# Kernel tuning notes

Measured on AMD Instinct MI355X. Metric: run time of the kernel, lower is better.

## Reference

```python
import jax, jax.numpy as jnp
import numpy as np

EPS = 1e-12
HEADS = 16
DIM_KEYS = 16
DIM_VALUES = 64


def l2norm(t):
    # matches F.normalize(t, p=2, dim=-1) with eps=1e-12
    n = jnp.linalg.norm(t, axis=-1, keepdims=True)
    return t / jnp.maximum(n, EPS)


def tanh_norm(t):
    n = jnp.linalg.norm(t, axis=-1, keepdims=True)
    return jnp.tanh(n) * (t / jnp.maximum(n, EPS))


def split_heads(x, h):
    # [b, n, h*d] -> [b, h, n, d]
    b, n, hd = x.shape
    return x.reshape(b, n, h, hd // h).transpose(0, 2, 1, 3)


def setup_inputs() -> dict:
    key = jax.random.key(0)
    k1, k2, k3, k4 = jax.random.split(key, 4)
    b, n, dim = 4, 2048, 1024
    dim_inner = (DIM_KEYS + DIM_VALUES) * HEADS  # 1280
    tokens = jax.random.normal(k1, (b, n, dim), dtype=jnp.float32)
    Wqg = jax.random.normal(k2, (dim, dim_inner), dtype=jnp.float32) * (dim ** -0.5)
    Wkv = jax.random.normal(k3, (dim, dim_inner), dtype=jnp.float32) * (dim ** -0.5)
    Wout = jax.random.normal(k4, (DIM_VALUES * HEADS, dim), dtype=jnp.float32) * ((DIM_VALUES * HEADS) ** -0.5)
    return {"tokens": tokens, "Wqg": Wqg, "Wkv": Wkv, "Wout": Wout}


def reference(tokens, Wqg, Wkv, Wout):
    # self-attention variant: context = tokens, mask = None
    qg = split_heads(tokens @ Wqg, HEADS)   # [b, h, n, dk+dv]
    kv = split_heads(tokens @ Wkv, HEADS)
    queries, gates = qg[..., :DIM_KEYS], qg[..., DIM_KEYS:]
    keys, values = kv[..., :DIM_KEYS], kv[..., DIM_KEYS:]
    queries, keys, values = l2norm(queries), l2norm(keys), l2norm(values)
    sim = jnp.einsum('bhid,bhjd->bhij', queries, keys)
    attn = jnp.square(jax.nn.relu(sim))
    aggr = jnp.einsum('bhij,bhjd->bhid', attn, values)
    out = tanh_norm(aggr) * jnp.tanh(jax.nn.silu(gates))
    b, h, n, d = out.shape
    out = out.transpose(0, 2, 1, 3).reshape(b, n, h * d)  # merge heads
    return out @ Wout
```

## Files before the change

### kernel.cpp

```cpp
#include <hip/hip_runtime.h>
#include <cstdint>
#include <cstddef>

typedef __attribute__((ext_vector_type(8))) short short8;
typedef __attribute__((ext_vector_type(8))) unsigned short ushort8;
typedef __attribute__((ext_vector_type(4))) float f32x4;
typedef __attribute__((ext_vector_type(8))) _Float16 half8;
typedef __attribute__((ext_vector_type(4))) _Float16 half4;
typedef __attribute__((ext_vector_type(2))) __fp16 fp16x2;

#define DEV static __device__ __forceinline__

DEV unsigned short f2bf(float x) {
  union { float f; unsigned u; } v; v.f = x;
  unsigned r = v.u + 0x7fffu + ((v.u >> 16) & 1u);
  return (unsigned short)(r >> 16);
}
DEV unsigned pack2bf(float lo, float hi) {
  union { float f; unsigned u; } a, b; a.f = lo; b.f = hi;
  return __builtin_amdgcn_perm(b.u + 0x8000u, a.u + 0x8000u, 0x07060302u);
}
DEV f32x4 mfma16(short8 a, short8 b, f32x4 c) {
  return __builtin_amdgcn_mfma_f32_16x16x32_bf16(a, b, c, 0, 0, 0);
}
DEV f32x4 mfma16h(half8 a, half8 b, f32x4 c) {
  return __builtin_amdgcn_mfma_f32_16x16x32_f16(a, b, c, 0, 0, 0);
}
DEV f32x4 mfma16k(half4 a, half4 b, f32x4 c) {
  return __builtin_amdgcn_mfma_f32_16x16x16f16(a, b, c, 0, 0, 0);
}

typedef __attribute__((address_space(1))) unsigned int g_u32;
typedef __attribute__((address_space(3))) unsigned int l_u32;
DEV void glds16(const unsigned short* g, unsigned short* l) {
  __builtin_amdgcn_global_load_lds((g_u32*)g, (l_u32*)l, 16, 0, 0);
}

constexpr int Bc = 4, Nc = 2048, Dc = 1024, Hc = 16, DKc = 16, DVc = 64, DIc = 1280;
constexpr int Mc = Bc * Nc;

__global__ __launch_bounds__(256) void prep_kernel(const float* __restrict__ X,
                                                   unsigned short* __restrict__ Xb,
                                                   const float* __restrict__ Wqg,
                                                   unsigned short* __restrict__ WqgT,
                                                   const float* __restrict__ Wkv,
                                                   unsigned short* __restrict__ WkvT,
                                                   const float* __restrict__ Wout,
                                                   unsigned short* __restrict__ WoutT) {
  __shared__ unsigned short tsh[64][72];
  int bid = blockIdx.x, tid = threadIdx.x;
  if (bid < 4096) {
    int i = bid * 256 + tid;
    const float4* p = (const float4*)(X + (size_t)i * 8);
    float4 a = p[0], b = p[1];
    ushort8 o;
    o[0] = f2bf(a.x); o[1] = f2bf(a.y); o[2] = f2bf(a.z); o[3] = f2bf(a.w);
    o[4] = f2bf(b.x); o[5] = f2bf(b.y); o[6] = f2bf(b.z); o[7] = f2bf(b.w);
    *(ushort8*)(Xb + (size_t)i * 8) = o;
    return;
  }
  const float* W; unsigned short* WT; int K, N, tb;
  if (bid < 4416)      { W = Wqg;  WT = WqgT;  K = Dc; N = DIc; tb = bid - 4096; }
  else if (bid < 4736) { W = Wkv;  WT = WkvT;  K = Dc; N = DIc; tb = bid - 4416; }
  else                 { W = Wout; WT = WoutT; K = Dc; N = Dc;  tb = bid - 4736; }
  int k0 = (tb & 15) * 64, n0 = (tb >> 4) * 64;
#pragma unroll
  for (int it = 0; it < 16; ++it) {
    int f = it * 256 + tid;
    int r = f >> 6, c = f & 63;
    tsh[c][r] = f2bf(W[(size_t)(k0 + r) * N + n0 + c]);
  }
  __syncthreads();
#pragma unroll
  for (int it = 0; it < 16; ++it) {
    int f = it * 256 + tid;
    int r = f >> 6, c = f & 63;
    WT[(size_t)(n0 + r) * K + k0 + c] = tsh[r][c];
  }
}

__global__ __launch_bounds__(256) void gemm_proj(const unsigned short* __restrict__ A,
                                                 const unsigned short* __restrict__ BT,
                                                 unsigned short* __restrict__ QG,
                                                 unsigned short* __restrict__ KV,
                                                 int Kq) {
  __shared__ unsigned short As[128 * 64];
  __shared__ unsigned short Bs[128 * 64];
  int L = blockIdx.x;
  int xcd = L & 7, idx = L >> 3;
  int brow = xcd * 8 + (idx & 7);
  int bcol = idx >> 3;
  int row0 = brow * 128, col0 = bcol * 128;
  int tid = threadIdx.x, lane = tid & 63, wave = tid >> 6;
  int wm = wave >> 1, wn = wave & 1;
  int ql = lane >> 4, l16 = lane & 15;
  int r8 = lane >> 3, cbl = (lane & 7) ^ r8;

  unsigned short* dst = (col0 >= DIc) ? KV : QG;
  int c0l = (col0 >= DIc) ? col0 - DIc : col0;

  const unsigned short* gA = A + (size_t)(row0 + wave * 32 + r8) * Kq + cbl * 8;
  const unsigned short* gB = BT + (size_t)(col0 + wave * 32 + r8) * Kq + cbl * 8;

  f32x4 acc[4][4];
#pragma unroll
  for (int i = 0; i < 4; i++)
#pragma unroll
    for (int j = 0; j < 4; j++) acc[i][j] = (f32x4){0.f, 0.f, 0.f, 0.f};

  for (int k0 = 0; k0 < Kq; k0 += 64) {
    __syncthreads();
#pragma unroll
    for (int i = 0; i < 4; ++i) {
      glds16(gA + (size_t)(i * 8) * Kq + k0, &As[(wave * 32 + i * 8) * 64]);
      glds16(gB + (size_t)(i * 8) * Kq + k0, &Bs[(wave * 32 + i * 8) * 64]);
    }
    __syncthreads();
#pragma unroll
    for (int kk = 0; kk < 64; kk += 32) {
      short8 af[4], bfr[4];
#pragma unroll
      for (int t = 0; t < 4; t++) {
        int row = wm * 64 + t * 16 + l16;
        int cb = (kk >> 3) + ql;
        af[t] = *(const short8*)&As[row * 64 + ((cb ^ (row & 7)) << 3)];
      }
#pragma unroll
      for (int t = 0; t < 4; t++) {
        int row = wn * 64 + t * 16 + l16;
        int cb = (kk >> 3) + ql;
        bfr[t] = *(const short8*)&Bs[row * 64 + ((cb ^ (row & 7)) << 3)];
      }
#pragma unroll
      for (int i = 0; i < 4; i++)
#pragma unroll
        for (int j = 0; j < 4; j++) acc[i][j] = mfma16(af[i], bfr[j], acc[i][j]);
    }
  }
#pragma unroll
  for (int i = 0; i < 4; i++)
#pragma unroll
    for (int j = 0; j < 4; j++)
#pragma unroll
      for (int r = 0; r < 4; r++) {
        int rr = row0 + wm * 64 + i * 16 + ql * 4 + r;
        int cc = c0l + wn * 64 + j * 16 + l16;
        union { _Float16 h; unsigned short us; } cv;
        cv.h = (_Float16)acc[i][j][r];
        dst[(size_t)rr * DIc + cc] = cv.us;
      }
}

__global__ __launch_bounds__(256) void gemm_glds(const unsigned short* __restrict__ A,
                                                 const unsigned short* __restrict__ BT,
                                                 float* __restrict__ Cout,
                                                 int Mq, int Nq, int Kq) {
  __shared__ unsigned short As[128 * 64];
  __shared__ unsigned short Bs[128 * 64];
  int L = blockIdx.x;
  int xcd = L & 7, idx = L >> 3;
  int brow = xcd * 8 + (idx & 7);
  int bcol = idx >> 3;
  int row0 = brow * 128, col0 = bcol * 128;
  int tid = threadIdx.x, lane = tid & 63, wave = tid >> 6;
  int wm = wave >> 1, wn = wave & 1;
  int ql = lane >> 4, l16 = lane & 15;
  int r8 = lane >> 3, cbl = (lane & 7) ^ r8;

  const unsigned short* gA = A + (size_t)(row0 + wave * 32 + r8) * Kq + cbl * 8;
  const unsigned short* gB = BT + (size_t)(col0 + wave * 32 + r8) * Kq + cbl * 8;

  f32x4 acc[4][4];
#pragma unroll
  for (int i = 0; i < 4; i++)
#pragma unroll
    for (int j = 0; j < 4; j++) acc[i][j] = (f32x4){0.f, 0.f, 0.f, 0.f};

  for (int k0 = 0; k0 < Kq; k0 += 64) {
    __syncthreads();
#pragma unroll
    for (int i = 0; i < 4; ++i) {
      glds16(gA + (size_t)(i * 8) * Kq + k0, &As[(wave * 32 + i * 8) * 64]);
      glds16(gB + (size_t)(i * 8) * Kq + k0, &Bs[(wave * 32 + i * 8) * 64]);
    }
    __syncthreads();
#pragma unroll
    for (int kk = 0; kk < 64; kk += 32) {
      short8 af[4], bfr[4];
#pragma unroll
      for (int t = 0; t < 4; t++) {
        int row = wm * 64 + t * 16 + l16;
        int cb = (kk >> 3) + ql;
        af[t] = *(const short8*)&As[row * 64 + ((cb ^ (row & 7)) << 3)];
      }
#pragma unroll
      for (int t = 0; t < 4; t++) {
        int row = wn * 64 + t * 16 + l16;
        int cb = (kk >> 3) + ql;
        bfr[t] = *(const short8*)&Bs[row * 64 + ((cb ^ (row & 7)) << 3)];
      }
#pragma unroll
      for (int i = 0; i < 4; i++)
#pragma unroll
        for (int j = 0; j < 4; j++) acc[i][j] = mfma16(af[i], bfr[j], acc[i][j]);
    }
  }
#pragma unroll
  for (int i = 0; i < 4; i++)
#pragma unroll
    for (int j = 0; j < 4; j++)
#pragma unroll
      for (int r = 0; r < 4; r++) {
        int rr = row0 + wm * 64 + i * 16 + ql * 4 + r;
        int cc = col0 + wn * 64 + j * 16 + l16;
        Cout[(size_t)rr * Nq + cc] = acc[i][j][r];
      }
}

__global__ __launch_bounds__(256) void norm_kernel(const unsigned short* __restrict__ QG,
                                                   const unsigned short* __restrict__ KV,
                                                   unsigned short* __restrict__ Qn,
                                                   unsigned short* __restrict__ Kn,
                                                   unsigned short* __restrict__ Vtg)
{
  int g = blockIdx.x * 256 + threadIdx.x;
  int n = g & (Nc - 1), bh = g >> 11;
  int h = bh & 15, b = bh >> 4;
  size_t src = ((size_t)(b * Nc + n)) * DIc + h * 80;

  {
    half8 u0 = *(const half8*)&QG[src];
    half8 u1 = *(const half8*)&QG[src + 8];
    float q[16], ss = 0.f;
#pragma unroll
    for (int i = 0; i < 8; i++) { q[i] = (float)u0[i]; q[8 + i] = (float)u1[i]; }
#pragma unroll
    for (int i = 0; i < 16; i++) ss += q[i] * q[i];
    float sc = 1.f / fmaxf(sqrtf(ss), 1e-12f);
    half8 o0, o1;
#pragma unroll
    for (int i = 0; i < 8; i++) { o0[i] = (_Float16)(q[i] * sc); o1[i] = (_Float16)(q[8 + i] * sc); }
    size_t dst = ((size_t)bh * Nc + n) * 16;
    *(half8*)&Qn[dst] = o0;
    *(half8*)&Qn[dst + 8] = o1;
  }
  {
    half8 u0 = *(const half8*)&KV[src];
    half8 u1 = *(const half8*)&KV[src + 8];
    float q[16], ss = 0.f;
#pragma unroll
    for (int i = 0; i < 8; i++) { q[i] = (float)u0[i]; q[8 + i] = (float)u1[i]; }
#pragma unroll
    for (int i = 0; i < 16; i++) ss += q[i] * q[i];
    float sc = 1.f / fmaxf(sqrtf(ss), 1e-12f);
    half8 o0, o1;
#pragma unroll
    for (int i = 0; i < 8; i++) { o0[i] = (_Float16)(q[i] * sc); o1[i] = (_Float16)(q[8 + i] * sc); }
    size_t dst = ((size_t)bh * Nc + n) * 16;
    *(half8*)&Kn[dst] = o0;
    *(half8*)&Kn[dst + 8] = o1;
  }
  {
    half8 u[8];
#pragma unroll
    for (int i = 0; i < 8; i++) u[i] = *(const half8*)&KV[src + 16 + i * 8];
    float ss = 0.f;
#pragma unroll
    for (int i = 0; i < 8; i++)
#pragma unroll
      for (int j = 0; j < 8; j++) { float x = (float)u[i][j]; ss += x * x; }
    float sc = 1.f / fmaxf(sqrtf(ss), 1e-12f);
#pragma unroll
    for (int i = 0; i < 8; i++)
#pragma unroll
      for (int j = 0; j < 8; j++) {
        int d = i * 8 + j;
        union { _Float16 h; unsigned short us; } cv;
        cv.h = (_Float16)((float)u[i][j] * sc);
        Vtg[((size_t)bh * DVc + d) * Nc + n] = cv.us;
      }
  }
}

__global__ __launch_bounds__(256, 4) void attn_kernel(const unsigned short* __restrict__ Qn,
                                                      const unsigned short* __restrict__ Kn,
                                                      const unsigned short* __restrict__ Vtg,
                                                      const unsigned short* __restrict__ QG,
                                                      unsigned short* __restrict__ outpre) {
  __shared__ unsigned short shm[2 * 64 * 128];

  int gid = blockIdx.x;
  int xcd = gid & 7, slot = gid >> 3;
  int bh = xcd * 8 + (slot & 7);
  int q0 = (slot >> 3) * 128;
  int b = bh >> 4, h = bh & 15;
  int tid = threadIdx.x, lane = tid & 63, wave = tid >> 6;
  int ql = lane >> 4, l16 = lane & 15;
  int qw0 = q0 + wave * 32;

  half4 qf[2];
#pragma unroll
  for (int qt = 0; qt < 2; ++qt)
    qf[qt] = *(const half4*)&Qn[((size_t)bh * Nc + qw0 + qt * 16 + l16) * 16 + ql * 4];

  const unsigned short* krow = Kn + (size_t)bh * Nc * 16;
  const unsigned short* vbase = Vtg + ((size_t)bh * DVc) * Nc;

  int lq = lane >> 4, m16 = lane & 15;

  f32x4 acc[4][2];
#pragma unroll
  for (int dt = 0; dt < 4; dt++) { acc[dt][0] = (f32x4){0.f,0.f,0.f,0.f}; acc[dt][1] = (f32x4){0.f,0.f,0.f,0.f}; }

  half4 kfA[8], kfB[8];

#pragma unroll
  for (int kh = 0; kh < 8; ++kh)
    kfA[kh] = *(const half4*)&krow[(size_t)(kh * 16 + l16) * 16 + ql * 4];
#pragma unroll
  for (int i = 0; i < 4; ++i) {
    int r0 = i * 16 + wave * 4;
    int d = r0 + lq;
    glds16(vbase + (size_t)d * Nc + 0 + ((m16 ^ (d & 7)) << 3), &shm[r0 * 128]);
  }

#define TILE_BODY(KT, KFU, KFN, LN)                                                      \
  {                                                                                      \
    __syncthreads();     \
    unsigned short* vtb = &shm[((KT) & 1) * 8192];                                       \
    if (LN) {                                                                            \
      int kn0 = ((KT) + 1) * 128;                                                        \
      unsigned short* nb = &shm[(((KT) + 1) & 1) * 8192];                                \
      _Pragma("unroll") for (int i = 0; i < 4; ++i) {                                    \
        int r0 = i * 16 + wave * 4;                                                      \
        int d = r0 + lq;                                                                 \
        glds16(vbase + (size_t)d * Nc + kn0 + ((m16 ^ (d & 7)) << 3), &nb[r0 * 128]);    \
      }                                                                                  \
      _Pragma("unroll") for (int kh = 0; kh < 8; ++kh)                                   \
        KFN[kh] = *(const half4*)&krow[(size_t)(kn0 + kh * 16 + l16) * 16 + ql * 4];     \
    }                                                                                    \
    _Pragma("unroll") for (int p = 0; p < 4; ++p) {                    \
      f32x4 c0[2], c1[2];                                                                \
      _Pragma("unroll") for (int qt = 0; qt < 2; ++qt) {                                 \
        c0[qt] = mfma16k(KFU[2 * p],     qf[qt], (f32x4){0.f, 0.f, 0.f, 0.f});           \
        c1[qt] = mfma16k(KFU[2 * p + 1], qf[qt], (f32x4){0.f, 0.f, 0.f, 0.f});           \
      }                                                                                  \
      half8 pf[2];                                                                       \
      _Pragma("unroll") for (int qt = 0; qt < 2; ++qt) {                                 \
        union { half8 hh; fp16x2 p2[4]; } w;                                             \
        fp16x2 t0 = __builtin_amdgcn_cvt_pkrtz(c0[qt][0], c0[qt][1]);                    \
        fp16x2 t1 = __builtin_amdgcn_cvt_pkrtz(c0[qt][2], c0[qt][3]);                    \
        fp16x2 t2 = __builtin_amdgcn_cvt_pkrtz(c1[qt][0], c1[qt][1]);                    \
        fp16x2 t3 = __builtin_amdgcn_cvt_pkrtz(c1[qt][2], c1[qt][3]);                    \
        const fp16x2 hz = {(__fp16)0, (__fp16)0};                                        \
        t0 = __builtin_elementwise_max(t0, hz); w.p2[0] = t0 * t0;                       \
        t1 = __builtin_elementwise_max(t1, hz); w.p2[1] = t1 * t1;                       \
        t2 = __builtin_elementwise_max(t2, hz); w.p2[2] = t2 * t2;                       \
        t3 = __builtin_elementwise_max(t3, hz); w.p2[3] = t3 * t3;                       \
        pf[qt] = w.hh;                                                                   \
      }                                                                                  \
               \
      int tsw = (l16 & 7) << 1;                                                          \
      int s1 = ((p * 8 + ql) ^ tsw) << 2;                                                \
      int s2 = ((p * 8 + 4 + ql) ^ tsw) << 2;                                            \
      __builtin_amdgcn_s_setprio(1);                                                     \
      _Pragma("unroll") for (int dt = 0; dt < 4; ++dt) {                                 \
        const unsigned short* vrow = vtb + (dt * 16 + l16) * 128;                        \
        union { half8 s; uint4 u; } vf;                                                  \
        uint2 va = *(const uint2*)&vrow[s1];                                             \
        uint2 vb2 = *(const uint2*)&vrow[s2];                                            \
        vf.u.x = va.x; vf.u.y = va.y; vf.u.z = vb2.x; vf.u.w = vb2.y;                    \
        _Pragma("unroll") for (int qt = 0; qt < 2; ++qt)                                 \
          acc[dt][qt] = mfma16h(vf.s, pf[qt], acc[dt][qt]);                              \
      }                                                                                  \
      __builtin_amdgcn_s_setprio(0);                                                     \
    }                                                                                    \
  }

#pragma unroll 1
  for (int kt2 = 0; kt2 < 8; ++kt2) {
    int kte = kt2 * 2;
    TILE_BODY(kte, kfA, kfB, 1)
    TILE_BODY(kte + 1, kfB, kfA, (kt2 < 7))
  }
#undef TILE_BODY

  __syncthreads();
  unsigned short(*of)[68] = (unsigned short(*)[68])shm;

#pragma unroll
  for (int qt = 0; qt < 2; ++qt) {
    float ss = 0.f;
#pragma unroll
    for (int dt = 0; dt < 4; ++dt)
#pragma unroll
      for (int r = 0; r < 4; ++r) { float v = acc[dt][qt][r]; ss += v * v; }
    ss += __shfl_xor(ss, 16, 64);
    ss += __shfl_xor(ss, 32, 64);
    float nrm = sqrtf(ss);
    float sc = tanhf(nrm) / fmaxf(nrm, 1e-12f);
    int q = qw0 + qt * 16 + l16;
    size_t gbase = ((size_t)(b * Nc + q)) * DIc + h * 80 + DKc;
#pragma unroll
    for (int dt = 0; dt < 4; ++dt) {
      uint2 gu = *(const uint2*)&QG[gbase + dt * 16 + ql * 4];
      union { uint2 u; _Float16 h[4]; } gv; gv.u = gu;
      float o[4];
#pragma unroll
      for (int r = 0; r < 4; ++r) {
        float x = (float)gv.h[r];
        float s = x / (1.f + __expf(-x));
        float e2 = __expf(2.f * s);
        float g = 1.f - 2.f / (e2 + 1.f);
        o[r] = acc[dt][qt][r] * sc * g;
      }
      uint2 w;
      w.x = pack2bf(o[0], o[1]);
      w.y = pack2bf(o[2], o[3]);
      *(uint2*)&of[wave * 32 + qt * 16 + l16][dt * 16 + ql * 4] = w;
    }
  }
  __syncthreads();
  {
    int row = tid >> 1, cb = (tid & 1) * 32;
    size_t obase = ((size_t)(b * Nc + q0 + row)) * (Hc * DVc) + h * DVc + cb;
#pragma unroll
    for (int i = 0; i < 4; ++i)
      *(ushort8*)&outpre[obase + i * 8] = *(const ushort8*)&of[row][cb + i * 8];
  }
}

extern "C" void kernel_launch(void* const* d_in, const int* in_sizes, int n_in,
                              void* d_out, int out_size, void* d_ws, size_t ws_size,
                              hipStream_t stream) {
  const float* X = (const float*)d_in[0];
  const float* Wqg = (const float*)d_in[1];
  const float* Wkv = (const float*)d_in[2];
  const float* Wout = (const float*)d_in[3];
  float* out = (float*)d_out;
  (void)in_sizes; (void)n_in; (void)out_size; (void)ws_size;

  char* ws = (char*)d_ws;
  size_t off = 0;
  auto alloc = [&](size_t bytes) {
    void* p = ws + off;
    off += (bytes + 255) & ~(size_t)255;
    return p;
  };
  unsigned short* Xbf   = (unsigned short*)alloc((size_t)Mc * Dc * 2);
  unsigned short* WqgT  = (unsigned short*)alloc((size_t)DIc * Dc * 2);
  unsigned short* WkvT  = (unsigned short*)alloc((size_t)DIc * Dc * 2);
  unsigned short* WoutT = (unsigned short*)alloc((size_t)Dc * Dc * 2);
  unsigned short* QG    = (unsigned short*)alloc((size_t)Mc * DIc * 2);
  unsigned short* KV    = (unsigned short*)alloc((size_t)Mc * DIc * 2);
  unsigned short* Qn    = (unsigned short*)alloc((size_t)Bc * Hc * Nc * 16 * 2);
  unsigned short* Kn    = (unsigned short*)alloc((size_t)Bc * Hc * Nc * 16 * 2);
  unsigned short* Vtg   = (unsigned short*)alloc((size_t)Bc * Hc * Nc * DVc * 2);
  unsigned short* outpre = Xbf;

  prep_kernel<<<4992, 256, 0, stream>>>(X, Xbf, Wqg, WqgT, Wkv, WkvT, Wout, WoutT);
  gemm_proj<<<Mc / 128 * (2 * DIc / 128), 256, 0, stream>>>(Xbf, WqgT, QG, KV, Dc);
  norm_kernel<<<(Mc * Hc) / 256, 256, 0, stream>>>(QG, KV, Qn, Kn, Vtg);
  attn_kernel<<<1024, 256, 0, stream>>>(Qn, Kn, Vtg, QG, outpre);
  gemm_glds<<<Mc / 128 * (Dc / 128), 256, 0, stream>>>(outpre, WoutT, out, Mc, Dc, Dc);
}
```

Before: 242.0 us.

## Use 8 waves per attention block with one query tile per wave

Result: slower. 264.7 us (+9.4%).

```diff
diff --git a/kernel.cpp b/kernel.cpp
--- a/kernel.cpp
+++ b/kernel.cpp
@@ -282,7 +282,7 @@
   }
 }
 
-__global__ __launch_bounds__(256, 4) void attn_kernel(const unsigned short* __restrict__ Qn,
+__global__ __launch_bounds__(512, 8) void attn_kernel(const unsigned short* __restrict__ Qn,
                                                       const unsigned short* __restrict__ Kn,
                                                       const unsigned short* __restrict__ Vtg,
                                                       const unsigned short* __restrict__ QG,
@@ -296,136 +296,120 @@
   int b = bh >> 4, h = bh & 15;
   int tid = threadIdx.x, lane = tid & 63, wave = tid >> 6;
   int ql = lane >> 4, l16 = lane & 15;
-  int qw0 = q0 + wave * 32;
-
-  half4 qf[2];
-#pragma unroll
-  for (int qt = 0; qt < 2; ++qt)
-    qf[qt] = *(const half4*)&Qn[((size_t)bh * Nc + qw0 + qt * 16 + l16) * 16 + ql * 4];
+  int qw0 = q0 + wave * 16;
+
+  half4 qf = *(const half4*)&Qn[((size_t)bh * Nc + qw0 + l16) * 16 + ql * 4];
 
   const unsigned short* krow = Kn + (size_t)bh * Nc * 16;
   const unsigned short* vbase = Vtg + ((size_t)bh * DVc) * Nc;
 
   int lq = lane >> 4, m16 = lane & 15;
-
-  f32x4 acc[4][2];
-#pragma unroll
-  for (int dt = 0; dt < 4; dt++) { acc[dt][0] = (f32x4){0.f,0.f,0.f,0.f}; acc[dt][1] = (f32x4){0.f,0.f,0.f,0.f}; }
-
-  half4 kfA[8], kfB[8];
-
-#pragma unroll
-  for (int kh = 0; kh < 8; ++kh)
-    kfA[kh] = *(const half4*)&krow[(size_t)(kh * 16 + l16) * 16 + ql * 4];
-#pragma unroll
-  for (int i = 0; i < 4; ++i) {
-    int r0 = i * 16 + wave * 4;
+  int tsw = (l16 & 7) << 1;
+
+  f32x4 acc[4];
+#pragma unroll
+  for (int dt = 0; dt < 4; dt++) acc[dt] = (f32x4){0.f, 0.f, 0.f, 0.f};
+
+#pragma unroll
+  for (int i = 0; i < 2; ++i) {
+    int r0 = i * 32 + wave * 4;
     int d = r0 + lq;
     glds16(vbase + (size_t)d * Nc + 0 + ((m16 ^ (d & 7)) << 3), &shm[r0 * 128]);
   }
 
-#define TILE_BODY(KT, KFU, KFN, LN)                                                      \
-  {                                                                                      \
-    __syncthreads();     \
-    unsigned short* vtb = &shm[((KT) & 1) * 8192];                                       \
-    if (LN) {                                                                            \
-      int kn0 = ((KT) + 1) * 128;                                                        \
-      unsigned short* nb = &shm[(((KT) + 1) & 1) * 8192];                                \
-      _Pragma("unroll") for (int i = 0; i < 4; ++i) {                                    \
-        int r0 = i * 16 + wave * 4;                                                      \
-        int d = r0 + lq;                                                                 \
-        glds16(vbase + (size_t)d * Nc + kn0 + ((m16 ^ (d & 7)) << 3), &nb[r0 * 128]);    \
-      }                                                                                  \
-      _Pragma("unroll") for (int kh = 0; kh < 8; ++kh)                                   \
-        KFN[kh] = *(const half4*)&krow[(size_t)(kn0 + kh * 16 + l16) * 16 + ql * 4];     \
-    }                                                                                    \
-    _Pragma("unroll") for (int p = 0; p < 4; ++p) {                    \
-      f32x4 c0[2], c1[2];                                                                \
-      _Pragma("unroll") for (int qt = 0; qt < 2; ++qt) {                                 \
-        c0[qt] = mfma16k(KFU[2 * p],     qf[qt], (f32x4){0.f, 0.f, 0.f, 0.f});           \
-        c1[qt] = mfma16k(KFU[2 * p + 1], qf[qt], (f32x4){0.f, 0.f, 0.f, 0.f});           \
-      }                                                                                  \
-      half8 pf[2];                                                                       \
-      _Pragma("unroll") for (int qt = 0; qt < 2; ++qt) {                                 \
-        union { half8 hh; fp16x2 p2[4]; } w;                                             \
-        fp16x2 t0 = __builtin_amdgcn_cvt_pkrtz(c0[qt][0], c0[qt][1]);                    \
-        fp16x2 t1 = __builtin_amdgcn_cvt_pkrtz(c0[qt][2], c0[qt][3]);                    \
-        fp16x2 t2 = __builtin_amdgcn_cvt_pkrtz(c1[qt][0], c1[qt][1]);                    \
-        fp16x2 t3 = __builtin_amdgcn_cvt_pkrtz(c1[qt][2], c1[qt][3]);                    \
-        const fp16x2 hz = {(__fp16)0, (__fp16)0};                                        \
-        t0 = __builtin_elementwise_max(t0, hz); w.p2[0] = t0 * t0;                       \
-        t1 = __builtin_elementwise_max(t1, hz); w.p2[1] = t1 * t1;                       \
-        t2 = __builtin_elementwise_max(t2, hz); w.p2[2] = t2 * t2;                       \
-        t3 = __builtin_elementwise_max(t3, hz); w.p2[3] = t3 * t3;                       \
-        pf[qt] = w.hh;                                                                   \
-      }                                                                                  \
-               \
-      int tsw = (l16 & 7) << 1;                                                          \
-      int s1 = ((p * 8 + ql) ^ tsw) << 2;                                                \
-      int s2 = ((p * 8 + 4 + ql) ^ tsw) << 2;                                            \
-      __builtin_amdgcn_s_setprio(1);                                                     \
-      _Pragma("unroll") for (int dt = 0; dt < 4; ++dt) {                                 \
-        const unsigned short* vrow = vtb + (dt * 16 + l16) * 128;                        \
-        union { half8 s; uint4 u; } vf;                                                  \
-        uint2 va = *(const uint2*)&vrow[s1];                                             \
-        uint2 vb2 = *(const uint2*)&vrow[s2];                                            \
-        vf.u.x = va.x; vf.u.y = va.y; vf.u.z = vb2.x; vf.u.w = vb2.y;                    \
-        _Pragma("unroll") for (int qt = 0; qt < 2; ++qt)                                 \
-          acc[dt][qt] = mfma16h(vf.s, pf[qt], acc[dt][qt]);                              \
-      }                                                                                  \
-      __builtin_amdgcn_s_setprio(0);                                                     \
-    }                                                                                    \
-  }
-
 #pragma unroll 1
-  for (int kt2 = 0; kt2 < 8; ++kt2) {
-    int kte = kt2 * 2;
-    TILE_BODY(kte, kfA, kfB, 1)
-    TILE_BODY(kte + 1, kfB, kfA, (kt2 < 7))
-  }
-#undef TILE_BODY
+  for (int kt = 0; kt < Nc / 128; ++kt) {
+    int k0 = kt * 128;
+    unsigned short* vtb = &shm[(kt & 1) * 8192];
+    __syncthreads();
+
+    half4 kf[8];
+#pragma unroll
+    for (int kh = 0; kh < 8; ++kh)
+      kf[kh] = *(const half4*)&krow[(size_t)(k0 + kh * 16 + l16) * 16 + ql * 4];
+
+    if (kt < Nc / 128 - 1) {
+      unsigned short* nb = &shm[((kt + 1) & 1) * 8192];
+      int kn0 = k0 + 128;
+#pragma unroll
+      for (int i = 0; i < 2; ++i) {
+        int r0 = i * 32 + wave * 4;
+        int d = r0 + lq;
+        glds16(vbase + (size_t)d * Nc + kn0 + ((m16 ^ (d & 7)) << 3), &nb[r0 * 128]);
+      }
+    }
+
+    __builtin_amdgcn_s_setprio(1);
+#pragma unroll
+    for (int p = 0; p < 4; ++p) {
+      f32x4 c0 = mfma16k(kf[2 * p],     qf, (f32x4){0.f, 0.f, 0.f, 0.f});
+      f32x4 c1 = mfma16k(kf[2 * p + 1], qf, (f32x4){0.f, 0.f, 0.f, 0.f});
+      union { half8 hh; fp16x2 p2[4]; } w;
+      fp16x2 t0 = __builtin_amdgcn_cvt_pkrtz(c0[0], c0[1]);
+      fp16x2 t1 = __builtin_amdgcn_cvt_pkrtz(c0[2], c0[3]);
+      fp16x2 t2 = __builtin_amdgcn_cvt_pkrtz(c1[0], c1[1]);
+      fp16x2 t3 = __builtin_amdgcn_cvt_pkrtz(c1[2], c1[3]);
+      const fp16x2 hz = {(__fp16)0, (__fp16)0};
+      t0 = __builtin_elementwise_max(t0, hz); w.p2[0] = t0 * t0;
+      t1 = __builtin_elementwise_max(t1, hz); w.p2[1] = t1 * t1;
+      t2 = __builtin_elementwise_max(t2, hz); w.p2[2] = t2 * t2;
+      t3 = __builtin_elementwise_max(t3, hz); w.p2[3] = t3 * t3;
+      half8 pf = w.hh;
+      int s1 = ((p * 8 + ql) ^ tsw) << 2;
+      int s2 = s1 ^ 16;
+#pragma unroll
+      for (int dt = 0; dt < 4; ++dt) {
+        const unsigned short* vrow = vtb + (dt * 16 + l16) * 128;
+        union { half8 s; uint4 u; } vf;
+        uint2 va = *(const uint2*)&vrow[s1];
+        uint2 vb2 = *(const uint2*)&vrow[s2];
+        vf.u.x = va.x; vf.u.y = va.y; vf.u.z = vb2.x; vf.u.w = vb2.y;
+        acc[dt] = mfma16h(vf.s, pf, acc[dt]);
+      }
+    }
+    __builtin_amdgcn_s_setprio(0);
+  }
 
   __syncthreads();
   unsigned short(*of)[68] = (unsigned short(*)[68])shm;
 
-#pragma unroll
-  for (int qt = 0; qt < 2; ++qt) {
+  {
     float ss = 0.f;
 #pragma unroll
     for (int dt = 0; dt < 4; ++dt)
 #pragma unroll
-      for (int r = 0; r < 4; ++r) { float v = acc[dt][qt][r]; ss += v * v; }
+      for (int r = 0; r < 4; ++r) { float v = acc[dt][r]; ss += v * v; }
     ss += __shfl_xor(ss, 16, 64);
     ss += __shfl_xor(ss, 32, 64);
     float nrm = sqrtf(ss);
     float sc = tanhf(nrm) / fmaxf(nrm, 1e-12f);
-    int q = qw0 + qt * 16 + l16;
+    int q = qw0 + l16;
     size_t gbase = ((size_t)(b * Nc + q)) * DIc + h * 80 + DKc;
 #pragma unroll
     for (int dt = 0; dt < 4; ++dt) {
       uint2 gu = *(const uint2*)&QG[gbase + dt * 16 + ql * 4];
-      union { uint2 u; _Float16 h[4]; } gv; gv.u = gu;
+      union { uint2 u; _Float16 hv[4]; } gv; gv.u = gu;
       float o[4];
 #pragma unroll
       for (int r = 0; r < 4; ++r) {
-        float x = (float)gv.h[r];
+        float x = (float)gv.hv[r];
         float s = x / (1.f + __expf(-x));
         float e2 = __expf(2.f * s);
         float g = 1.f - 2.f / (e2 + 1.f);
-        o[r] = acc[dt][qt][r] * sc * g;
+        o[r] = acc[dt][r] * sc * g;
       }
       uint2 w;
       w.x = pack2bf(o[0], o[1]);
       w.y = pack2bf(o[2], o[3]);
-      *(uint2*)&of[wave * 32 + qt * 16 + l16][dt * 16 + ql * 4] = w;
+      *(uint2*)&of[wave * 16 + l16][dt * 16 + ql * 4] = w;
     }
   }
   __syncthreads();
   {
-    int row = tid >> 1, cb = (tid & 1) * 32;
+    int row = tid >> 2, cb = (tid & 3) * 16;
     size_t obase = ((size_t)(b * Nc + q0 + row)) * (Hc * DVc) + h * DVc + cb;
 #pragma unroll
-    for (int i = 0; i < 4; ++i)
+    for (int i = 0; i < 2; ++i)
       *(ushort8*)&outpre[obase + i * 8] = *(const ushort8*)&of[row][cb + i * 8];
   }
 }
@@ -461,6 +445,6 @@
   prep_kernel<<<4992, 256, 0, stream>>>(X, Xbf, Wqg, WqgT, Wkv, WkvT, Wout, WoutT);
   gemm_proj<<<Mc / 128 * (2 * DIc / 128), 256, 0, stream>>>(Xbf, WqgT, QG, KV, Dc);
   norm_kernel<<<(Mc * Hc) / 256, 256, 0, stream>>>(QG, KV, Qn, Kn, Vtg);
-  attn_kernel<<<1024, 256, 0, stream>>>(Qn, Kn, Vtg, QG, outpre);
+  attn_kernel<<<1024, 512, 0, stream>>>(Qn, Kn, Vtg, QG, outpre);
   gemm_glds<<<Mc / 128 * (Dc / 128), 256, 0, stream>>>(outpre, WoutT, out, Mc, Dc, Dc);
 }
```

## Double per-block query tile in attention to reuse K/V tiles across more queries

Applied to the files above, without the earlier changes.

Result: slower. 294.2 us (+21.6%).

```diff
diff --git a/kernel.cpp b/kernel.cpp
--- a/kernel.cpp
+++ b/kernel.cpp
@@ -282,7 +282,7 @@
   }
 }
 
-__global__ __launch_bounds__(256, 4) void attn_kernel(const unsigned short* __restrict__ Qn,
+__global__ __launch_bounds__(256, 2) void attn_kernel(const unsigned short* __restrict__ Qn,
                                                       const unsigned short* __restrict__ Kn,
                                                       const unsigned short* __restrict__ Vtg,
                                                       const unsigned short* __restrict__ QG,
@@ -292,25 +292,28 @@
   int gid = blockIdx.x;
   int xcd = gid & 7, slot = gid >> 3;
   int bh = xcd * 8 + (slot & 7);
-  int q0 = (slot >> 3) * 128;
+  int q0 = (slot >> 3) * 256;
   int b = bh >> 4, h = bh & 15;
   int tid = threadIdx.x, lane = tid & 63, wave = tid >> 6;
   int ql = lane >> 4, l16 = lane & 15;
-  int qw0 = q0 + wave * 32;
-
-  half4 qf[2];
-#pragma unroll
-  for (int qt = 0; qt < 2; ++qt)
+  int qw0 = q0 + wave * 64;
+
+  half4 qf[4];
+#pragma unroll
+  for (int qt = 0; qt < 4; ++qt)
     qf[qt] = *(const half4*)&Qn[((size_t)bh * Nc + qw0 + qt * 16 + l16) * 16 + ql * 4];
 
   const unsigned short* krow = Kn + (size_t)bh * Nc * 16;
   const unsigned short* vbase = Vtg + ((size_t)bh * DVc) * Nc;
 
   int lq = lane >> 4, m16 = lane & 15;
-
-  f32x4 acc[4][2];
-#pragma unroll
-  for (int dt = 0; dt < 4; dt++) { acc[dt][0] = (f32x4){0.f,0.f,0.f,0.f}; acc[dt][1] = (f32x4){0.f,0.f,0.f,0.f}; }
+  int tsw = (l16 & 7) << 1;
+
+  f32x4 acc[4][4];
+#pragma unroll
+  for (int dt = 0; dt < 4; dt++)
+#pragma unroll
+    for (int qt = 0; qt < 4; qt++) acc[dt][qt] = (f32x4){0.f, 0.f, 0.f, 0.f};
 
   half4 kfA[8], kfB[8];
 
@@ -339,14 +342,15 @@
       _Pragma("unroll") for (int kh = 0; kh < 8; ++kh)                                   \
         KFN[kh] = *(const half4*)&krow[(size_t)(kn0 + kh * 16 + l16) * 16 + ql * 4];     \
     }                                                                                    \
+    __builtin_amdgcn_s_setprio(1);                                                       \
     _Pragma("unroll") for (int p = 0; p < 4; ++p) {                    \
-      f32x4 c0[2], c1[2];                                                                \
-      _Pragma("unroll") for (int qt = 0; qt < 2; ++qt) {                                 \
+      f32x4 c0[4], c1[4];                                                                \
+      _Pragma("unroll") for (int qt = 0; qt < 4; ++qt) {                                 \
         c0[qt] = mfma16k(KFU[2 * p],     qf[qt], (f32x4){0.f, 0.f, 0.f, 0.f});           \
         c1[qt] = mfma16k(KFU[2 * p + 1], qf[qt], (f32x4){0.f, 0.f, 0.f, 0.f});           \
       }                                                                                  \
-      half8 pf[2];                                                                       \
-      _Pragma("unroll") for (int qt = 0; qt < 2; ++qt) {                                 \
+      half8 pf[4];                                                                       \
+      _Pragma("unroll") for (int qt = 0; qt < 4; ++qt) {                                 \
         union { half8 hh; fp16x2 p2[4]; } w;                                             \
         fp16x2 t0 = __builtin_amdgcn_cvt_pkrtz(c0[qt][0], c0[qt][1]);                    \
         fp16x2 t1 = __builtin_amdgcn_cvt_pkrtz(c0[qt][2], c0[qt][3]);                    \
@@ -359,22 +363,20 @@
         t3 = __builtin_elementwise_max(t3, hz); w.p2[3] = t3 * t3;                       \
         pf[qt] = w.hh;                                                                   \
       }                                                                                  \
-               \
-      int tsw = (l16 & 7) << 1;                                                          \
+                                      \
       int s1 = ((p * 8 + ql) ^ tsw) << 2;                                                \
-      int s2 = ((p * 8 + 4 + ql) ^ tsw) << 2;                                            \
-      __builtin_amdgcn_s_setprio(1);                                                     \
+      int s2 = s1 ^ 16;                                                                  \
       _Pragma("unroll") for (int dt = 0; dt < 4; ++dt) {                                 \
         const unsigned short* vrow = vtb + (dt * 16 + l16) * 128;                        \
         union { half8 s; uint4 u; } vf;                                                  \
         uint2 va = *(const uint2*)&vrow[s1];                                             \
         uint2 vb2 = *(const uint2*)&vrow[s2];                                            \
         vf.u.x = va.x; vf.u.y = va.y; vf.u.z = vb2.x; vf.u.w = vb2.y;                    \
-        _Pragma("unroll") for (int qt = 0; qt < 2; ++qt)                                 \
+        _Pragma("unroll") for (int qt = 0; qt < 4; ++qt)                                 \
           acc[dt][qt] = mfma16h(vf.s, pf[qt], acc[dt][qt]);                              \
       }                                                                                  \
-      __builtin_amdgcn_s_setprio(0);                                                     \
     }                                                                                    \
+    __builtin_amdgcn_s_setprio(0);                                                       \
   }
 
 #pragma unroll 1
@@ -385,48 +387,55 @@
   }
 #undef TILE_BODY
 
-  __syncthreads();
   unsigned short(*of)[68] = (unsigned short(*)[68])shm;
-
-#pragma unroll
-  for (int qt = 0; qt < 2; ++qt) {
-    float ss = 0.f;
-#pragma unroll
-    for (int dt = 0; dt < 4; ++dt)
-#pragma unroll
-      for (int r = 0; r < 4; ++r) { float v = acc[dt][qt][r]; ss += v * v; }
-    ss += __shfl_xor(ss, 16, 64);
-    ss += __shfl_xor(ss, 32, 64);
-    float nrm = sqrtf(ss);
-    float sc = tanhf(nrm) / fmaxf(nrm, 1e-12f);
-    int q = qw0 + qt * 16 + l16;
-    size_t gbase = ((size_t)(b * Nc + q)) * DIc + h * 80 + DKc;
-#pragma unroll
-    for (int dt = 0; dt < 4; ++dt) {
-      uint2 gu = *(const uint2*)&QG[gbase + dt * 16 + ql * 4];
-      union { uint2 u; _Float16 h[4]; } gv; gv.u = gu;
-      float o[4];
-#pragma unroll
-      for (int r = 0; r < 4; ++r) {
-        float x = (float)gv.h[r];
-        float s = x / (1.f + __expf(-x));
-        float e2 = __expf(2.f * s);
-        float g = 1.f - 2.f / (e2 + 1.f);
-        o[r] = acc[dt][qt][r] * sc * g;
-      }
-      uint2 w;
-      w.x = pack2bf(o[0], o[1]);
-      w.y = pack2bf(o[2], o[3]);
-      *(uint2*)&of[wave * 32 + qt * 16 + l16][dt * 16 + ql * 4] = w;
-    }
-  }
-  __syncthreads();
-  {
-    int row = tid >> 1, cb = (tid & 1) * 32;
-    size_t obase = ((size_t)(b * Nc + q0 + row)) * (Hc * DVc) + h * DVc + cb;
-#pragma unroll
-    for (int i = 0; i < 4; ++i)
-      *(ushort8*)&outpre[obase + i * 8] = *(const ushort8*)&of[row][cb + i * 8];
+#pragma unroll 1
+  for (int hh = 0; hh < 2; ++hh) {
+    __syncthreads();
+#pragma unroll
+    for (int qi = 0; qi < 2; ++qi) {
+      float ss = 0.f;
+#pragma unroll
+      for (int dt = 0; dt < 4; ++dt)
+#pragma unroll
+        for (int r = 0; r < 4; ++r) {
+          float v = (qi == 0) ? acc[dt][2 * hh][r] : acc[dt][2 * hh + 1][r];
+          ss += v * v;
+        }
+      ss += __shfl_xor(ss, 16, 64);
+      ss += __shfl_xor(ss, 32, 64);
+      float nrm = sqrtf(ss);
+      float sc = tanhf(nrm) / fmaxf(nrm, 1e-12f);
+      int q = qw0 + (hh * 2 + qi) * 16 + l16;
+      size_t gbase = ((size_t)(b * Nc + q)) * DIc + h * 80 + DKc;
+#pragma unroll
+      for (int dt = 0; dt < 4; ++dt) {
+        uint2 gu = *(const uint2*)&QG[gbase + dt * 16 + ql * 4];
+        union { uint2 u; _Float16 hv[4]; } gv; gv.u = gu;
+        float o[4];
+#pragma unroll
+        for (int r = 0; r < 4; ++r) {
+          float x = (float)gv.hv[r];
+          float av = (qi == 0) ? acc[dt][2 * hh][r] : acc[dt][2 * hh + 1][r];
+          float s = x / (1.f + __expf(-x));
+          float e2 = __expf(2.f * s);
+          float g = 1.f - 2.f / (e2 + 1.f);
+          o[r] = av * sc * g;
+        }
+        uint2 w;
+        w.x = pack2bf(o[0], o[1]);
+        w.y = pack2bf(o[2], o[3]);
+        *(uint2*)&of[wave * 32 + qi * 16 + l16][dt * 16 + ql * 4] = w;
+      }
+    }
+    __syncthreads();
+    {
+      int row = tid >> 1, cb = (tid & 1) * 32;
+      int q = q0 + (row >> 5) * 64 + hh * 32 + (row & 31);
+      size_t obase = ((size_t)(b * Nc + q)) * (Hc * DVc) + h * DVc + cb;
+#pragma unroll
+      for (int i = 0; i < 4; ++i)
+        *(ushort8*)&outpre[obase + i * 8] = *(const ushort8*)&of[row][cb + i * 8];
+    }
   }
 }
 
@@ -461,6 +470,6 @@
   prep_kernel<<<4992, 256, 0, stream>>>(X, Xbf, Wqg, WqgT, Wkv, WkvT, Wout, WoutT);
   gemm_proj<<<Mc / 128 * (2 * DIc / 128), 256, 0, stream>>>(Xbf, WqgT, QG, KV, Dc);
   norm_kernel<<<(Mc * Hc) / 256, 256, 0, stream>>>(QG, KV, Qn, Kn, Vtg);
-  attn_kernel<<<1024, 256, 0, stream>>>(Qn, Kn, Vtg, QG, outpre);
+  attn_kernel<<<512, 256, 0, stream>>>(Qn, Kn, Vtg, QG, outpre);
   gemm_glds<<<Mc / 128 * (Dc / 128), 256, 0, stream>>>(outpre, WoutT, out, Mc, Dc, Dc);
 }
```
